# Kernel tuning notes

Measured on AMD Instinct MI355X. Metric: run time of the kernel, lower is better.

## Reference

```python
import jax, jax.numpy as jnp
import numpy as np

NUM_SPHERICAL = 7
NUM_RADIAL = 6
CUTOFF = 5.0
ENVELOPE_EXPONENT = 5
ENVELOPE_CUTOFF = 5.0  # hardcoded in the torch module: poly_envelop(cutoff=5.0, ...)
E = 1_000_000   # num edges
T = 4_000_000   # num triplets (angles)


def _jn_np(l, x):
    """Spherical Bessel j_l(x) in numpy via upward recurrence (x > 0)."""
    j0 = np.sin(x) / x
    if l == 0:
        return j0
    j1 = np.sin(x) / x ** 2 - np.cos(x) / x
    for i in range(2, l + 1):
        j0, j1 = j1, (2 * i - 1) / x * j1 - j0
    return j1


def _jn_zeros(n, k):
    """First k positive zeros of j_l for l=0..n-1 (zeros interlace)."""
    zeros = np.zeros((n, k))
    prev = np.arange(1, k + n) * np.pi  # zeros of j_0
    zeros[0] = prev[:k]
    for l in range(1, n):
        cur = []
        for i in range(len(prev) - 1):
            a, b = prev[i], prev[i + 1]
            fa = _jn_np(l, a)
            for _ in range(80):  # bisection
                m = 0.5 * (a + b)
                fm = _jn_np(l, m)
                if np.sign(fm) == np.sign(fa):
                    a, fa = m, fm
                else:
                    b = m
            cur.append(0.5 * (a + b))
        prev = np.array(cur)
        zeros[l] = prev[:k]
    return zeros


# constants derived from (num_spherical, num_radial) at build time
Z = _jn_zeros(NUM_SPHERICAL, NUM_RADIAL)  # [S, R] Bessel zeros z_{l,n}
NORM = np.array([[np.sqrt(2.0) / abs(_jn_np(l + 1, Z[l, n])) for n in range(NUM_RADIAL)]
                 for l in range(NUM_SPHERICAL)])  # [S, R]
Y_NORM = np.array([np.sqrt((2 * l + 1) / (4.0 * np.pi)) for l in range(NUM_SPHERICAL)])  # m=0 SH norms


def _spherical_jn(l, a):
    """j_l(a) in jax via upward recurrence."""
    j0 = jnp.sin(a) / a
    if l == 0:
        return j0
    j1 = jnp.sin(a) / a ** 2 - jnp.cos(a) / a
    for i in range(2, l + 1):
        j0, j1 = j1, (2 * i - 1) / a * j1 - j0
    return j1


def _envelope(d):
    """DimeNet polynomial envelope, p = exponent + 1, on u = d / cutoff."""
    p = ENVELOPE_EXPONENT + 1
    a = -(p + 1) * (p + 2) / 2.0
    b = float(p * (p + 2))
    c = -p * (p + 1) / 2.0
    u = d / ENVELOPE_CUTOFF
    env = 1.0 / u + a * u ** (p - 1) + b * u ** p + c * u ** (p + 1)
    return jnp.where(u < 1.0, env, 0.0)


def setup_inputs() -> dict:
    key = jax.random.key(0)
    k1, k2, k3 = jax.random.split(key, 3)
    d = jax.random.uniform(k1, (E,), jnp.float32, 0.5, CUTOFF)           # edge distances
    Angles = jax.random.uniform(k2, (T,), jnp.float32, 0.0, float(np.pi))  # triplet angles
    edge_index_1 = jax.random.randint(k3, (T,), 0, E, dtype=jnp.int64 if jax.config.jax_enable_x64 else jnp.int32)
    return {"d": d, "Angles": Angles, "edge_index_1": edge_index_1}


def reference(d, Angles, edge_index_1):
    S, R = NUM_SPHERICAL, NUM_RADIAL
    zeros = jnp.asarray(Z, d.dtype)     # [S, R]
    norm = jnp.asarray(NORM, d.dtype)   # [S, R]
    x = d / CUTOFF                      # [E]
    # radial basis: norm_{l,n} * j_l(z_{l,n} * x)  -> [E, S, R]
    rbf = jnp.stack([norm[l] * _spherical_jn(l, zeros[l][None, :] * x[:, None])
                     for l in range(S)], axis=1)
    rbf_env = (_envelope(d)[:, None, None] * rbf).reshape(d.shape[0], S * R)  # [E, S*R]
    rbf_env = rbf_env[edge_index_1]  # gather triplets -> [T, S*R]
    # angular basis: Y_l^0(theta) = sqrt((2l+1)/4pi) * P_l(cos theta)
    c = jnp.cos(Angles)
    P = [jnp.ones_like(c), c]
    for l in range(2, S):
        P.append(((2 * l - 1) * c * P[l - 1] - (l - 1) * P[l - 2]) / l)
    y_norm = jnp.asarray(Y_NORM, c.dtype)
    cbf = jnp.stack([y_norm[l] * P[l] for l in range(S)], axis=1)  # [T, S]
    cbf = jnp.repeat(cbf, R, axis=1)  # repeat_interleave -> [T, S*R]
    return rbf_env * cbf
```

## Files before the change

kernel.cpp:

```cpp
#include <hip/hip_runtime.h>
#include <hip/hip_bf16.h>
#include <hip/hip_fp16.h>
#include <math.h>

#define NSPH 7
#define NRAD 6
#define NJ 42
#define ROWH 44
#define BLK 256

typedef float v2f __attribute__((ext_vector_type(2)));

struct KC {
  float zf[NJ];
  float izf[NJ];
  float nyf[NJ];
  float sc5[7];
  float sc6[7];
};

__global__ void __launch_bounds__(BLK, 4) k_fused(const float* __restrict__ d,
                                                  const float* __restrict__ ang,
                                                  const int* __restrict__ idx,
                                                  float* __restrict__ out,
                                                  int T, KC C) {
  __shared__ __half sv[BLK * ROWH];
  const int tid = threadIdx.x;
  const int t0 = blockIdx.x * BLK;
  const int t = t0 + tid;

  if (t < T) {
    const int e = __builtin_nontemporal_load(idx + t);
    const float an = __builtin_nontemporal_load(ang + t);
    const float dv = d[e];

    const float x = dv / 5.0f;
    const float invx = 1.0f / x;
    const float x2 = x * x;
    const float x5 = x2 * x2 * x;
    float env = invx + x5 * fmaf(x, fmaf(x, -21.0f, 48.0f), -28.0f);
    if (x >= 1.0f) env = 0.0f;

    const float cth = __cosf(an);
    float mP[NSPH];
    {
      float p0 = 1.f, p1 = cth;
      mP[0] = env; mP[1] = env * cth;
      const float rl[5] = {1.f/2.f, 1.f/3.f, 1.f/4.f, 1.f/5.f, 1.f/6.f};
      #pragma unroll
      for (int l = 2; l < NSPH; ++l) {
        float pn = (fmaf((float)(2*l-1) * cth, p1, -(float)(l-1) * p0)) * rl[l-2];
        mP[l] = env * pn;
        p0 = p1; p1 = pn;
      }
    }

    __half* row = sv + tid * ROWH;

    #pragma unroll
    for (int l = 0; l < 5; ++l) {
      float jv[NRAD];
      #pragma unroll
      for (int n = 0; n < NRAD; ++n) {
        const int i = l * NRAD + n;
        float a = C.zf[i] * x;
        float s = __sinf(a);
        float inva = C.izf[i] * invx;
        float j0 = s * inva;
        float jl;
        if (l == 0) {
          jl = j0;
        } else {
          float c = __cosf(a);
          float j1 = (j0 - c) * inva;
          #pragma unroll
          for (int m = 2; m <= l; ++m) {
            float jn_ = fmaf((float)(2*m-1) * inva, j1, -j0);
            j0 = j1; j1 = jn_;
          }
          jl = j1;
        }
        jv[n] = (C.nyf[i] * jl) * mP[l];
      }
      __half2* dst = (__half2*)(row + l * NRAD);
      dst[0] = __float22half2_rn((float2){jv[0], jv[1]});
      dst[1] = __float22half2_rn((float2){jv[2], jv[3]});
      dst[2] = __float22half2_rn((float2){jv[4], jv[5]});
    }

    #pragma unroll
    for (int l = 5; l < NSPH; ++l) {
      const float* sc = (l == 5) ? C.sc5 : C.sc6;
      float jv[NRAD];
      #pragma unroll
      for (int n = 0; n < NRAD; ++n) {
        const int i = l * NRAD + n;
        float a = C.zf[i] * x;
        float inva = C.izf[i] * invx;
        float s = __sinf(a);
        float c = __cosf(a);
        float j0 = s * inva;
        float j1 = (j0 - c) * inva;
        #pragma unroll
        for (int m = 2; m <= l; ++m) {
          float jn_ = fmaf((float)(2*m-1) * inva, j1, -j0);
          j0 = j1; j1 = jn_;
        }
        float u = a * a;
        float p = fmaf(u, sc[6], sc[5]);
        p = fmaf(u, p, sc[4]);
        p = fmaf(u, p, sc[3]);
        p = fmaf(u, p, sc[2]);
        p = fmaf(u, p, sc[1]);
        p = fmaf(u, p, sc[0]);
        float u2 = u * u;
        float al = (l == 5) ? (u2 * a) : (u2 * u);
        float jser = al * p;
        float jl = (a < 4.0f) ? jser : j1;
        jv[n] = (C.nyf[i] * jl) * mP[l];
      }
      __half2* dst = (__half2*)(row + l * NRAD);
      dst[0] = __float22half2_rn((float2){jv[0], jv[1]});
      dst[1] = __float22half2_rn((float2){jv[2], jv[3]});
      dst[2] = __float22half2_rn((float2){jv[4], jv[5]});
    }
  }
  __syncthreads();

  v2f* obase = (v2f*)(out + (size_t)t0 * NJ);
  #pragma unroll
  for (int k = 0; k < 21; ++k) {
    unsigned w = k * BLK + tid;
    unsigned tl = w / 21u;
    unsigned jp = w - tl * 21u;
    if ((int)(t0 + tl) < T) {
      __half2 hh = *(const __half2*)(sv + tl * ROWH + 2 * jp);
      float2 r = __half22float2(hh);
      __builtin_nontemporal_store((v2f){r.x, r.y}, obase + w);
    }
  }
}

static double jn_host(int l, double x) {
  double j0 = sin(x) / x;
  if (l == 0) return j0;
  double j1 = sin(x) / (x * x) - cos(x) / x;
  for (int i = 2; i <= l; ++i) {
    double jn_ = (2 * i - 1) / x * j1 - j0;
    j0 = j1; j1 = jn_;
  }
  return j1;
}

extern "C" void kernel_launch(void* const* d_in, const int* in_sizes, int n_in,
                              void* d_out, int out_size, void* d_ws, size_t ws_size,
                              hipStream_t stream) {
  const float* d   = (const float*)d_in[0];
  const float* ang = (const float*)d_in[1];
  const int*   idx = (const int*)d_in[2];
  float* out = (float*)d_out;
  const int T = in_sizes[1];

  KC C;
  {
    const double PI = 3.14159265358979323846;
    double zeros[NSPH][NRAD];
    double prev[NSPH + NRAD - 1];
    int np_ = NSPH + NRAD - 1;
    for (int i = 0; i < np_; ++i) prev[i] = (i + 1) * PI;
    for (int j = 0; j < NRAD; ++j) zeros[0][j] = prev[j];
    for (int l = 1; l < NSPH; ++l) {
      int nc = np_ - 1;
      double cur[NSPH + NRAD - 1];
      for (int i = 0; i < nc; ++i) {
        double a = prev[i], b = prev[i + 1];
        double fa = jn_host(l, a);
        for (int it = 0; it < 80; ++it) {
          double m = 0.5 * (a + b);
          double fm = jn_host(l, m);
          if ((fm > 0.0) == (fa > 0.0)) { a = m; fa = fm; } else { b = m; }
        }
        cur[i] = 0.5 * (a + b);
      }
      for (int i = 0; i < nc; ++i) prev[i] = cur[i];
      np_ = nc;
      for (int j = 0; j < NRAD; ++j) zeros[l][j] = prev[j];
    }
    for (int l = 0; l < NSPH; ++l) {
      double yn = sqrt((2.0 * l + 1.0) / (4.0 * PI));
      for (int n = 0; n < NRAD; ++n) {
        int i = l * NRAD + n;
        double z = zeros[l][n];
        C.zf[i]  = (float)z;
        C.izf[i] = (float)(1.0 / z);
        C.nyf[i] = (float)(sqrt(2.0) / fabs(jn_host(l + 1, z)) * yn);
      }
    }
    for (int l = 5; l <= 6; ++l) {
      double dfact = 1.0;
      for (int m = 2 * l + 1; m > 1; m -= 2) dfact *= m;
      double ck = 1.0 / dfact;
      float* sc = (l == 5) ? C.sc5 : C.sc6;
      sc[0] = (float)ck;
      for (int k = 1; k < 7; ++k) {
        ck = -ck / (2.0 * k * (2 * l + 2 * k + 1));
        sc[k] = (float)ck;
      }
    }
  }

  k_fused<<<(T + BLK - 1) / BLK, BLK, 0, stream>>>(d, ang, idx, out, T, C);
}
```

Baseline: 171.1 us.

## Vectorize Bessel evaluation in float2 pairs, use fast rcp, plain output stores

Rewrites the per-radial Bessel computation to handle two radial indices at a time with float2 vector types, so the compiler can emit packed FP32 math (v_pk_fma/v_pk_mul). It also swaps the division by 5 and the reciprocal for a multiply and the hardware rcp intrinsic. The final output stores change from nontemporal to ordinary stores. The kernel writes a large output, so it is likely bound by memory writes, and the ALU savings may not matter much. Dropping the nontemporal hint could change cache behaviour on the writeback.

```diff
diff --git a/kernel.cpp b/kernel.cpp
--- a/kernel.cpp
+++ b/kernel.cpp
@@ -9,7 +9,7 @@
 #define ROWH 44
 #define BLK 256
 
-typedef float v2f __attribute__((ext_vector_type(2)));
+typedef float v2 __attribute__((ext_vector_type(2)));
 
 struct KC {
   float zf[NJ];
@@ -34,8 +34,8 @@
     const float an = __builtin_nontemporal_load(ang + t);
     const float dv = d[e];
 
-    const float x = dv / 5.0f;
-    const float invx = 1.0f / x;
+    const float x = dv * 0.2f;
+    const float invx = __builtin_amdgcn_rcpf(x);
     const float x2 = x * x;
     const float x5 = x2 * x2 * x;
     float env = invx + x5 * fmaf(x, fmaf(x, -21.0f, 48.0f), -28.0f);
@@ -59,75 +59,75 @@
 
     #pragma unroll
     for (int l = 0; l < 5; ++l) {
-      float jv[NRAD];
       #pragma unroll
-      for (int n = 0; n < NRAD; ++n) {
-        const int i = l * NRAD + n;
-        float a = C.zf[i] * x;
-        float s = __sinf(a);
-        float inva = C.izf[i] * invx;
-        float j0 = s * inva;
-        float jl;
+      for (int p = 0; p < 3; ++p) {
+        const int i = l * NRAD + 2 * p;
+        v2 z    = {C.zf[i],  C.zf[i+1]};
+        v2 iz   = {C.izf[i], C.izf[i+1]};
+        v2 ny   = {C.nyf[i], C.nyf[i+1]};
+        v2 a    = z * x;
+        v2 s;  s.x = __sinf(a.x);  s.y = __sinf(a.y);
+        v2 inva = iz * invx;
+        v2 j0   = s * inva;
+        v2 jl;
         if (l == 0) {
           jl = j0;
         } else {
-          float c = __cosf(a);
-          float j1 = (j0 - c) * inva;
+          v2 c;  c.x = __cosf(a.x);  c.y = __cosf(a.y);
+          v2 j1 = (j0 - c) * inva;
           #pragma unroll
           for (int m = 2; m <= l; ++m) {
-            float jn_ = fmaf((float)(2*m-1) * inva, j1, -j0);
+            v2 jn_ = ((float)(2*m-1) * inva) * j1 - j0;
             j0 = j1; j1 = jn_;
           }
           jl = j1;
         }
-        jv[n] = (C.nyf[i] * jl) * mP[l];
-      }
-      __half2* dst = (__half2*)(row + l * NRAD);
-      dst[0] = __float22half2_rn((float2){jv[0], jv[1]});
-      dst[1] = __float22half2_rn((float2){jv[2], jv[3]});
-      dst[2] = __float22half2_rn((float2){jv[4], jv[5]});
+        v2 jv = (ny * jl) * mP[l];
+        *(__half2*)(row + i) = __float22half2_rn((float2){jv.x, jv.y});
+      }
     }
 
     #pragma unroll
     for (int l = 5; l < NSPH; ++l) {
       const float* sc = (l == 5) ? C.sc5 : C.sc6;
-      float jv[NRAD];
       #pragma unroll
-      for (int n = 0; n < NRAD; ++n) {
-        const int i = l * NRAD + n;
-        float a = C.zf[i] * x;
-        float inva = C.izf[i] * invx;
-        float s = __sinf(a);
-        float c = __cosf(a);
-        float j0 = s * inva;
-        float j1 = (j0 - c) * inva;
+      for (int p = 0; p < 3; ++p) {
+        const int i = l * NRAD + 2 * p;
+        v2 z    = {C.zf[i],  C.zf[i+1]};
+        v2 iz   = {C.izf[i], C.izf[i+1]};
+        v2 ny   = {C.nyf[i], C.nyf[i+1]};
+        v2 a    = z * x;
+        v2 s;  s.x = __sinf(a.x);  s.y = __sinf(a.y);
+        v2 c;  c.x = __cosf(a.x);  c.y = __cosf(a.y);
+        v2 inva = iz * invx;
+        v2 j0   = s * inva;
+        v2 j1   = (j0 - c) * inva;
         #pragma unroll
         for (int m = 2; m <= l; ++m) {
-          float jn_ = fmaf((float)(2*m-1) * inva, j1, -j0);
+          v2 jn_ = ((float)(2*m-1) * inva) * j1 - j0;
           j0 = j1; j1 = jn_;
         }
-        float u = a * a;
-        float p = fmaf(u, sc[6], sc[5]);
-        p = fmaf(u, p, sc[4]);
-        p = fmaf(u, p, sc[3]);
-        p = fmaf(u, p, sc[2]);
-        p = fmaf(u, p, sc[1]);
-        p = fmaf(u, p, sc[0]);
-        float u2 = u * u;
-        float al = (l == 5) ? (u2 * a) : (u2 * u);
-        float jser = al * p;
-        float jl = (a < 4.0f) ? jser : j1;
-        jv[n] = (C.nyf[i] * jl) * mP[l];
-      }
-      __half2* dst = (__half2*)(row + l * NRAD);
-      dst[0] = __float22half2_rn((float2){jv[0], jv[1]});
-      dst[1] = __float22half2_rn((float2){jv[2], jv[3]});
-      dst[2] = __float22half2_rn((float2){jv[4], jv[5]});
+        v2 u  = a * a;
+        v2 pp = u * sc[6] + sc[5];
+        pp = u * pp + sc[4];
+        pp = u * pp + sc[3];
+        pp = u * pp + sc[2];
+        pp = u * pp + sc[1];
+        pp = u * pp + sc[0];
+        v2 u2 = u * u;
+        v2 al = (l == 5) ? (u2 * a) : (u2 * u);
+        v2 jser = al * pp;
+        v2 jl;
+        jl.x = (a.x < 4.0f) ? jser.x : j1.x;
+        jl.y = (a.y < 4.0f) ? jser.y : j1.y;
+        v2 jv = (ny * jl) * mP[l];
+        *(__half2*)(row + i) = __float22half2_rn((float2){jv.x, jv.y});
+      }
     }
   }
   __syncthreads();
 
-  v2f* obase = (v2f*)(out + (size_t)t0 * NJ);
+  v2* obase = (v2*)(out + (size_t)t0 * NJ);
   #pragma unroll
   for (int k = 0; k < 21; ++k) {
     unsigned w = k * BLK + tid;
@@ -136,7 +136,7 @@
     if ((int)(t0 + tl) < T) {
       __half2 hh = *(const __half2*)(sv + tl * ROWH + 2 * jp);
       float2 r = __half22float2(hh);
-      __builtin_nontemporal_store((v2f){r.x, r.y}, obase + w);
+      obase[w] = (v2){r.x, r.y};
     }
   }
 }
```

New measurement: 177.6 us. 1.04x slower.
